# Kernel tuning notes

Hardware: AMD Instinct MI355X
Metric: run time of the kernel (lower is better)

The kernel has to match this reference:

```python
import math
import jax, jax.numpy as jnp
import numpy as np

B, T, D, NH = 4, 2048, 1024, 16
HS = D // NH
N_BUCKETS = 32
MAX_DIST = 128


def _relative_position_bucket(rp):
    # bidirectional T5 bucketing, n_buckets=32, max_distance=128
    nb = N_BUCKETS // 2  # 16
    buckets = (rp > 0).astype(jnp.int32) * nb
    rp = jnp.abs(rp)
    max_exact = nb // 2  # 8
    is_small = rp < max_exact
    me = max_exact - 1   # 7
    nbm = nb - 1         # 15
    rp_safe = jnp.maximum(rp, 1).astype(jnp.float32)
    rp_large = me + (jnp.log(rp_safe / me) / math.log(MAX_DIST / me) * (nbm - me)).astype(jnp.int32)
    rp_large = jnp.minimum(rp_large, nbm)
    buckets = buckets + jnp.where(is_small, rp, rp_large)
    return buckets


def compute_bias(rel_emb, qT, kT):
    ctx = jnp.arange(qT, dtype=jnp.int32)[:, None]
    mem = jnp.arange(kT, dtype=jnp.int32)[None, :]
    bucket = _relative_position_bucket(mem - ctx)  # [qT, kT]
    values = rel_emb[bucket]                        # [qT, kT, NH]
    return jnp.transpose(values, (2, 0, 1))[None]   # [1, NH, qT, kT]


def setup_inputs() -> dict:
    key = jax.random.key(0)
    ks = jax.random.split(key, 6)
    s = 0.02
    return {
        "queries": jax.random.normal(ks[0], (B, T, D), jnp.float32),
        "Wq": jax.random.normal(ks[1], (D, D), jnp.float32) * s,
        "Wk": jax.random.normal(ks[2], (D, D), jnp.float32) * s,
        "Wv": jax.random.normal(ks[3], (D, D), jnp.float32) * s,
        "Wo": jax.random.normal(ks[4], (D, D), jnp.float32) * s,
        "rel_emb": jax.random.normal(ks[5], (N_BUCKETS, NH), jnp.float32) * s,
    }


def reference(queries, Wq, Wk, Wv, Wo, rel_emb):
    b, t, d = queries.shape
    def split_heads(x):
        return jnp.transpose(x.reshape(b, t, NH, HS), (0, 2, 1, 3))  # [B, nh, T, hs]
    q = split_heads(queries @ Wq.T)
    k = split_heads(queries @ Wk.T)
    v = split_heads(queries @ Wv.T)
    att = jnp.einsum('bhqd,bhkd->bhqk', q, k) * (1.0 / math.sqrt(HS))
    att = att + compute_bias(rel_emb, t, t)
    att = jax.nn.softmax(att, axis=-1)
    o = jnp.einsum('bhqk,bhkd->bhqd', att, v)
    o = jnp.transpose(o, (0, 2, 1, 3)).reshape(b, t, d)
    return o @ Wo.T
```

## Files before the change

### kernel.cpp

```cpp
#include <hip/hip_runtime.h>
#include <math.h>

#define T_SEQ 2048
#define D_MODEL 1024
#define NHEADS 16
#define HSZ 64
#define BATCH 4

typedef __bf16 bf16x8 __attribute__((ext_vector_type(8)));
typedef __bf16 bf16x4 __attribute__((ext_vector_type(4)));
typedef short short4v __attribute__((ext_vector_type(4)));
typedef float f32x4 __attribute__((ext_vector_type(4)));
typedef float f32x16 __attribute__((ext_vector_type(16)));

__device__ __forceinline__ unsigned short f2bf(float f) {
    unsigned int u = __builtin_bit_cast(unsigned int, f);
    u += 0x7fff + ((u >> 16) & 1);
    return (unsigned short)(u >> 16);
}

__device__ __forceinline__ unsigned int pk2bf(float a, float b) {
#if __has_builtin(__builtin_amdgcn_cvt_pk_bf16_f32)
    typedef __bf16 bf16x2_t __attribute__((ext_vector_type(2)));
    bf16x2_t v = __builtin_amdgcn_cvt_pk_bf16_f32(a, b);
    return __builtin_bit_cast(unsigned int, v);
#else
    return (unsigned int)f2bf(a) | ((unsigned int)f2bf(b) << 16);
#endif
}

__device__ __forceinline__ float fexp2(float x) {
#if __has_builtin(__builtin_amdgcn_exp2f)
    return __builtin_amdgcn_exp2f(x);
#else
    return __builtin_exp2f(x);
#endif
}

__device__ __forceinline__ void pl32swap(unsigned int& a, unsigned int& b) {
#if __has_builtin(__builtin_amdgcn_permlane32_swap)
    auto r = __builtin_amdgcn_permlane32_swap((int)a, (int)b, false, false);
    a = (unsigned int)r[0];
    b = (unsigned int)r[1];
#else
    unsigned int sa = (unsigned int)__shfl_xor((int)a, 32);
    unsigned int sb = (unsigned int)__shfl_xor((int)b, 32);
    const int hi = (int)((threadIdx.x & 63) >> 5);
    unsigned int na = hi ? sb : a;
    unsigned int nb = hi ? b : sa;
    a = na; b = nb;
#endif
}

__device__ __forceinline__ void gld_lds16(const void* g, void* lds) {
    __builtin_amdgcn_global_load_lds(
        (const __attribute__((address_space(1))) unsigned int*)g,
        (__attribute__((address_space(3))) unsigned int*)lds, 16, 0, 0);
}

__device__ __forceinline__ bf16x8 ld8(const unsigned short* p) {
    return *(const bf16x8*)p;
}

__device__ __forceinline__ float t5_bias(int delta, int h, const float* __restrict__ rel) {
    int bucket = delta > 0 ? 16 : 0;
    int arp = delta < 0 ? -delta : delta;
    if (arp < 8) {
        bucket += arp;
    } else {
        float f = logf((float)arp / 7.0f) * (8.0f / logf(128.0f / 7.0f));
        int rl = 7 + (int)f;
        bucket += rl < 15 ? rl : 15;
    }
    return rel[bucket * NHEADS + h] * 1.4426950408889634f;
}

__global__ void prep(const float* __restrict__ x,
                     const float* __restrict__ w0, const float* __restrict__ w1,
                     const float* __restrict__ w2, const float* __restrict__ w3,
                     unsigned short* __restrict__ Xbf,
                     unsigned short* __restrict__ Wbf) {
    int bid = blockIdx.x;
    int tid = threadIdx.x;
    if (bid < 8192) {
        int i = bid * 256 + tid;
        float4 v = ((const float4*)x)[i];
        ushort4 o;
        o.x = f2bf(v.x); o.y = f2bf(v.y); o.z = f2bf(v.z); o.w = f2bf(v.w);
        ((ushort4*)Xbf)[i] = o;
    } else {
        int wsel = (bid - 8192) >> 10;
        const float* srcs[4] = {w0, w1, w2, w3};
        int i = ((bid - 8192) & 1023) * 256 + tid;
        float4 v = ((const float4*)srcs[wsel])[i];
        ushort4 o;
        o.x = f2bf(v.x); o.y = f2bf(v.y); o.z = f2bf(v.z); o.w = f2bf(v.w);
        ((ushort4*)(Wbf + (size_t)wsel * 1048576))[i] = o;
    }
}

template<int MODE>
__global__ __launch_bounds__(256, 2) void gemm_bt(
    const unsigned short* __restrict__ A,
    const unsigned short* __restrict__ Bw,
    void* __restrict__ out)
{
    constexpr int K = 1024;
    __shared__ __align__(16) char smem[36864];
    unsigned short* As = (unsigned short*)smem;
    unsigned short* Bs = (unsigned short*)(smem + 16384);

    const int tid  = threadIdx.x;
    const int wave = tid >> 6;
    const int lane = tid & 63;
    const int quad = lane >> 4;
    const int l16  = lane & 15;
    const int wm   = wave >> 1;
    const int wn   = wave & 1;
    const int bn   = blockIdx.x;
    const int bm   = blockIdx.y;

    const int r_in = lane >> 3;
    const int lc   = (lane & 7) ^ r_in;

    f32x4 acc[4][4];
    #pragma unroll
    for (int m = 0; m < 4; ++m)
        #pragma unroll
        for (int n = 0; n < 4; ++n)
            acc[m][n] = f32x4{0.f, 0.f, 0.f, 0.f};

    const long a_row0 = (long)bm * 128;
    const long b_row0 = (long)bn * 128;

    for (int kt = 0; kt < K / 64; ++kt) {
        __syncthreads();
        const int k0 = kt * 64 + lc * 8;
        #pragma unroll
        for (int c = 0; c < 4; ++c) {
            int cc = wave * 4 + c;
            int r  = cc * 8 + r_in;
            gld_lds16(A  + (a_row0 + r) * K + k0, &As[cc * 512]);
            gld_lds16(Bw + (b_row0 + r) * K + k0, &Bs[cc * 512]);
        }
        __syncthreads();

        bf16x8 af[4][2], bf[4][2];
        #pragma unroll
        for (int m = 0; m < 4; ++m)
            #pragma unroll
            for (int ks = 0; ks < 2; ++ks) {
                int r  = wm * 64 + m * 16 + l16;
                int pc = (ks * 4 + quad) ^ (r & 7);
                af[m][ks] = ld8(&As[r * 64 + pc * 8]);
            }
        #pragma unroll
        for (int n = 0; n < 4; ++n)
            #pragma unroll
            for (int ks = 0; ks < 2; ++ks) {
                int r  = wn * 64 + n * 16 + l16;
                int pc = (ks * 4 + quad) ^ (r & 7);
                bf[n][ks] = ld8(&Bs[r * 64 + pc * 8]);
            }
        #pragma unroll
        for (int ks = 0; ks < 2; ++ks)
            #pragma unroll
            for (int m = 0; m < 4; ++m)
                #pragma unroll
                for (int n = 0; n < 4; ++n)
                    acc[m][n] = __builtin_amdgcn_mfma_f32_16x16x32_bf16(
                        af[m][ks], bf[n][ks], acc[m][n], 0, 0, 0);
    }

    const int which = (MODE == 4) ? (bn >> 3) : 0;
    if (MODE == 3) {
        float* O = (float*)out;
        #pragma unroll
        for (int m = 0; m < 4; ++m) {
            int row = bm * 128 + wm * 64 + m * 16 + quad * 4;
            #pragma unroll
            for (int n = 0; n < 4; ++n) {
                int col = bn * 128 + wn * 64 + n * 16 + l16;
                #pragma unroll
                for (int r = 0; r < 4; ++r)
                    O[(long)(row + r) * 1024 + col] = acc[m][n][r];
            }
        }
    } else if (which == 2) {
        unsigned short* O = (unsigned short*)out + (size_t)2 * 8388608;
        #pragma unroll
        for (int m = 0; m < 4; ++m) {
            int row = bm * 128 + wm * 64 + m * 16 + quad * 4;
            int b = row >> 11, t = row & 2047;
            #pragma unroll
            for (int n = 0; n < 4; ++n) {
                int cl = (bn * 128 + wn * 64 + n * 16 + l16) & 1023;
                int h = cl >> 6, hs = cl & 63;
                ushort4 pk;
                pk.x = f2bf(acc[m][n][0]); pk.y = f2bf(acc[m][n][1]);
                pk.z = f2bf(acc[m][n][2]); pk.w = f2bf(acc[m][n][3]);
                *(ushort4*)&O[(long)((b * 16 + h) * 64 + hs) * 2048 + t] = pk;
            }
        }
    } else {
        __syncthreads();
        unsigned short* Ew = (unsigned short*)smem + wave * 4608;
        const float qs = (which == 0) ? 0.125f * 1.4426950408889634f : 1.0f;
        #pragma unroll
        for (int m = 0; m < 4; ++m)
            #pragma unroll
            for (int n = 0; n < 4; ++n)
                #pragma unroll
                for (int r = 0; r < 4; ++r)
                    Ew[(m * 16 + quad * 4 + r) * 72 + n * 16 + l16] =
                        f2bf(acc[m][n][r] * qs);
        asm volatile("s_waitcnt lgkmcnt(0)" ::: "memory");

        const int cl0 = (bn * 128 + wn * 64) & 1023;
        const int h   = cl0 >> 6;
        const int gr0 = bm * 128 + wm * 64;
        const int b   = gr0 >> 11, t0 = gr0 & 2047;
        unsigned short* O = (unsigned short*)out + (size_t)which * 8388608
                          + ((size_t)(b * 16 + h) * 2048 + t0) * 64;
        #pragma unroll
        for (int rr = 0; rr < 8; ++rr) {
            int row   = rr * 8 + (lane >> 3);
            int chunk = lane & 7;
            uint4 v = *(const uint4*)&Ew[row * 72 + chunk * 8];
            *(uint4*)&O[(size_t)row * 64 + chunk * 8] = v;
        }
    }
}

__global__ __launch_bounds__(256, 4) void attn(
    const unsigned short* __restrict__ Q,
    const unsigned short* __restrict__ Kb,
    const unsigned short* __restrict__ Vt,
    const float* __restrict__ rel,
    unsigned short* __restrict__ AO)
{
    __shared__ __align__(16) char smem[33824];
    unsigned short* KsB = (unsigned short*)smem;
    unsigned short* VsB = (unsigned short*)(smem + 16384);
    float*          Bb  = (float*)(smem + 32768);

    const int tid  = threadIdx.x;
    const int wave = tid >> 6;
    const int lane = tid & 63;
    const int l31  = lane & 31;
    const int h5   = lane >> 5;

    const int bh = blockIdx.y;
    const int b  = bh >> 4, h = bh & 15;
    const int q0 = blockIdx.x * 128;

    const unsigned short* Qg = Q  + (long)bh * T_SEQ * HSZ;
    const unsigned short* Kg = Kb + (long)bh * T_SEQ * HSZ;
    const unsigned short* Vg = Vt + (long)bh * HSZ * T_SEQ;

    const int r_in = lane >> 3;
    const int lc   = (lane & 7) ^ r_in;

    {
        #pragma unroll
        for (int c = 0; c < 2; ++c) {
            int cc = wave * 2 + c;
            int r  = cc * 8 + r_in;
            gld_lds16(Kg + (long)r * 64 + lc * 8, &KsB[cc * 512]);
            gld_lds16(Vg + (long)r * T_SEQ + lc * 8, &VsB[cc * 512]);
        }
    }

    for (int i = tid; i < 263; i += 256)
        Bb[i] = t5_bias(i - 131, h, rel);

    const int qrow_lane = q0 + wave * 32 + l31;
    bf16x8 qf[4];
    #pragma unroll
    for (int hsc = 0; hsc < 4; ++hsc)
        qf[hsc] = ld8(&Qg[(long)qrow_lane * 64 + hsc * 16 + h5 * 8]);

    f32x16 o0 = {0.f,0.f,0.f,0.f,0.f,0.f,0.f,0.f,0.f,0.f,0.f,0.f,0.f,0.f,0.f,0.f};
    f32x16 o1 = o0;
    float li = 0.0f;

    const float cneg = rel[15 * NHEADS + h] * 1.4426950408889634f;
    const float cpos = rel[31 * NHEADS + h] * 1.4426950408889634f;

    for (int kt = 0; kt < T_SEQ / 64; ++kt) {
        const int cur = kt & 1;
        __syncthreads();

        if (kt + 1 < T_SEQ / 64) {
            unsigned short* Kn = KsB + (cur ^ 1) * 4096;
            unsigned short* Vn = VsB + (cur ^ 1) * 4096;
            #pragma unroll
            for (int c = 0; c < 2; ++c) {
                int cc = wave * 2 + c;
                int r  = cc * 8 + r_in;
                gld_lds16(Kg + (long)((kt + 1) * 64 + r) * 64 + lc * 8, &Kn[cc * 512]);
                gld_lds16(Vg + (long)r * T_SEQ + (kt + 1) * 64 + lc * 8, &Vn[cc * 512]);
            }
        }

        const unsigned short* Ks = KsB + cur * 4096;
        const unsigned short* Vs = VsB + cur * 4096;

        const int lo = kt * 64 - q0 - 127;
        const int hi = kt * 64 + 63 - q0;
        const bool outband = (lo >= 128) || (hi <= -128);
        const float cb = (lo >= 128) ? cpos : cneg;

        #pragma unroll
        for (int tt = 0; tt < 2; ++tt) {
            const int rk = tt * 32 + l31;
            bf16x8 af[4];
            #pragma unroll
            for (int hsc = 0; hsc < 4; ++hsc)
                af[hsc] = ld8(&Ks[rk * 64 + (((hsc << 1) | h5) ^ (rk & 7)) * 8]);

            f32x16 s;
            if (outband) {
                #pragma unroll
                for (int e = 0; e < 16; ++e) s[e] = cb;
            } else {
                const int ibase = kt * 64 + tt * 32 + h5 * 4 + 131 - qrow_lane;
                #pragma unroll
                for (int g = 0; g < 4; ++g) {
                    int i0 = ibase + g * 8;
                    i0 = i0 < 0 ? 0 : (i0 > 259 ? 259 : i0);
                    #pragma unroll
                    for (int r = 0; r < 4; ++r) s[g * 4 + r] = Bb[i0 + r];
                }
            }

            __builtin_amdgcn_s_setprio(1);
            #pragma unroll
            for (int hsc = 0; hsc < 4; ++hsc)
                s = __builtin_amdgcn_mfma_f32_32x32x16_bf16(af[hsc], qf[hsc], s, 0, 0, 0);
            __builtin_amdgcn_s_setprio(0);

            float p[16];
            #pragma unroll
            for (int e = 0; e < 16; ++e) p[e] = fexp2(s[e]);
            {
                float t0 = (p[0]  + p[1])  + (p[2]  + p[3]);
                float t1 = (p[4]  + p[5])  + (p[6]  + p[7]);
                float t2 = (p[8]  + p[9])  + (p[10] + p[11]);
                float t3 = (p[12] + p[13]) + (p[14] + p[15]);
                li += (t0 + t1) + (t2 + t3);
            }

            unsigned int x0 = pk2bf(p[0],  p[1]),  x1 = pk2bf(p[2],  p[3]);
            unsigned int y0 = pk2bf(p[4],  p[5]),  y1 = pk2bf(p[6],  p[7]);
            unsigned int z0 = pk2bf(p[8],  p[9]),  z1 = pk2bf(p[10], p[11]);
            unsigned int u0 = pk2bf(p[12], p[13]), u1 = pk2bf(p[14], p[15]);
            pl32swap(x0, y0); pl32swap(x1, y1);
            pl32swap(z0, u0); pl32swap(z1, u1);
            uint4 pw0 = {x0, x1, y0, y1};
            uint4 pw1 = {z0, z1, u0, u1};
            bf16x8 pf[2] = {__builtin_bit_cast(bf16x8, pw0),
                            __builtin_bit_cast(bf16x8, pw1)};

            #pragma unroll
            for (int c = 0; c < 2; ++c) {
                const int tc = tt * 2 + c;
                const int rv0 = l31;
                const int rv1 = 32 + l31;
                bf16x8 vf0 = ld8(&Vs[rv0 * 64 + (((tc << 1) | h5) ^ (rv0 & 7)) * 8]);
                bf16x8 vf1 = ld8(&Vs[rv1 * 64 + (((tc << 1) | h5) ^ (rv1 & 7)) * 8]);
                __builtin_amdgcn_s_setprio(1);
                o0 = __builtin_amdgcn_mfma_f32_32x32x16_bf16(pf[c], vf0, o0, 0, 0, 0);
                o1 = __builtin_amdgcn_mfma_f32_32x32x16_bf16(pf[c], vf1, o1, 0, 0, 0);
                __builtin_amdgcn_s_setprio(0);
            }
        }
    }

    li += __shfl_xor(li, 32);
    const float inv = 1.0f / li;

    #pragma unroll
    for (int g = 0; g < 4; ++g) {
        #pragma unroll
        for (int r = 0; r < 4; ++r) {
            const int ql = g * 8 + h5 * 4 + r;
            const float iv = __shfl(inv, ql);
            const int qrow = q0 + wave * 32 + ql;
            unsigned short* dst =
                &AO[(long)(b * T_SEQ + qrow) * D_MODEL + h * 64 + l31];
            dst[0]  = f2bf(o0[g * 4 + r] * iv);
            dst[32] = f2bf(o1[g * 4 + r] * iv);
        }
    }
}

extern "C" void kernel_launch(void* const* d_in, const int* in_sizes, int n_in,
                              void* d_out, int out_size, void* d_ws, size_t ws_size,
                              hipStream_t stream) {
    const float* x   = (const float*)d_in[0];
    const float* wq  = (const float*)d_in[1];
    const float* wk  = (const float*)d_in[2];
    const float* wv  = (const float*)d_in[3];
    const float* wo  = (const float*)d_in[4];
    const float* rel = (const float*)d_in[5];

    char* ws = (char*)d_ws;
    unsigned short* Xbf = (unsigned short*)(ws);
    unsigned short* Wbf = (unsigned short*)(ws + (16l << 20));
    unsigned short* Qb  = (unsigned short*)(ws + (24l << 20));

    prep<<<12288, 256, 0, stream>>>(x, wq, wk, wv, wo, Xbf, Wbf);

    gemm_bt<4><<<dim3(24, 64), 256, 0, stream>>>(Xbf, Wbf, Qb);

    unsigned short* Kbf = Qb + 8388608;
    unsigned short* Vtb = Qb + 16777216;
    unsigned short* AO  = Xbf;
    attn<<<dim3(16, 64), 256, 0, stream>>>(Qb, Kbf, Vtb, rel, AO);

    gemm_bt<3><<<dim3(8, 64), 256, 0, stream>>>(AO, Wbf + 3 * 1048576, d_out);
}
```

Before: 283.6 us.

## Double-buffer GEMM LDS tiles and swizzle workgroups across XCDs

The bf16 GEMM kernel gets two LDS buffers, 64KB in total. The next K-tile's global-to-LDS loads are issued before computing on the current tile, so memory latency overlaps with MFMA work, and one barrier per iteration is removed. Workgroup IDs are also remapped so that consecutive blocks on the same XCD share A/B rows, which should improve L2 reuse. The larger LDS footprint could cap occupancy, and the remap assumes a fixed grid shape per MODE.

After: 272.3 us. 1.04x faster.

```diff
diff --git a/kernel.cpp b/kernel.cpp
--- a/kernel.cpp
+++ b/kernel.cpp
@@ -106,9 +106,7 @@
     void* __restrict__ out)
 {
     constexpr int K = 1024;
-    __shared__ __align__(16) char smem[36864];
-    unsigned short* As = (unsigned short*)smem;
-    unsigned short* Bs = (unsigned short*)(smem + 16384);
+    __shared__ __align__(16) char smem[65536];
 
     const int tid  = threadIdx.x;
     const int wave = tid >> 6;
@@ -117,8 +115,13 @@
     const int l16  = lane & 15;
     const int wm   = wave >> 1;
     const int wn   = wave & 1;
-    const int bn   = blockIdx.x;
-    const int bm   = blockIdx.y;
+
+    constexpr int NWGX = (MODE == 4) ? 24 : 8;
+    const int orig = blockIdx.x + blockIdx.y * NWGX;
+    constexpr int CPX = (NWGX * 64) / 8;
+    const int swz  = (orig & 7) * CPX + (orig >> 3);
+    const int bn   = swz % NWGX;
+    const int bm   = swz / NWGX;
 
     const int r_in = lane >> 3;
     const int lc   = (lane & 7) ^ r_in;
@@ -133,17 +136,38 @@
     const long a_row0 = (long)bm * 128;
     const long b_row0 = (long)bn * 128;
 
-    for (int kt = 0; kt < K / 64; ++kt) {
-        __syncthreads();
-        const int k0 = kt * 64 + lc * 8;
+    {
+        const int k0 = lc * 8;
+        unsigned short* As_ = (unsigned short*)smem;
+        unsigned short* Bs_ = (unsigned short*)(smem + 16384);
         #pragma unroll
         for (int c = 0; c < 4; ++c) {
             int cc = wave * 4 + c;
             int r  = cc * 8 + r_in;
-            gld_lds16(A  + (a_row0 + r) * K + k0, &As[cc * 512]);
-            gld_lds16(Bw + (b_row0 + r) * K + k0, &Bs[cc * 512]);
-        }
+            gld_lds16(A  + (a_row0 + r) * K + k0, &As_[cc * 512]);
+            gld_lds16(Bw + (b_row0 + r) * K + k0, &Bs_[cc * 512]);
+        }
+    }
+
+    for (int kt = 0; kt < K / 64; ++kt) {
+        const int cur = kt & 1;
         __syncthreads();
+
+        if (kt + 1 < K / 64) {
+            const int k0 = (kt + 1) * 64 + lc * 8;
+            unsigned short* As_ = (unsigned short*)(smem + (cur ^ 1) * 32768);
+            unsigned short* Bs_ = (unsigned short*)(smem + (cur ^ 1) * 32768 + 16384);
+            #pragma unroll
+            for (int c = 0; c < 4; ++c) {
+                int cc = wave * 4 + c;
+                int r  = cc * 8 + r_in;
+                gld_lds16(A  + (a_row0 + r) * K + k0, &As_[cc * 512]);
+                gld_lds16(Bw + (b_row0 + r) * K + k0, &Bs_[cc * 512]);
+            }
+        }
+
+        unsigned short* As = (unsigned short*)(smem + cur * 32768);
+        unsigned short* Bs = (unsigned short*)(smem + cur * 32768 + 16384);
 
         bf16x8 af[4][2], bf[4][2];
         #pragma unroll
```
